# Performance work log

Hardware: AMD Instinct MI355X
Metric: run time of the kernel (lower is better)

The kernel has to match this reference:

```python
import jax, jax.numpy as jnp
import numpy as np
import math

D_MODEL = 1024
H = 16
D_H = D_MODEL // H
B, T = 1, 4096


def setup_inputs() -> dict:
    key = jax.random.key(0)
    ks = jax.random.split(key, 9)
    s = 1.0 / math.sqrt(D_MODEL)
    return {
        "x": jax.random.normal(ks[0], (B, T, D_MODEL), dtype=jnp.float32),
        "W_q": jax.random.normal(ks[1], (D_MODEL, D_MODEL), dtype=jnp.float32) * s,
        "b_q": jax.random.normal(ks[2], (D_MODEL,), dtype=jnp.float32) * 0.01,
        "W_k": jax.random.normal(ks[3], (D_MODEL, D_MODEL), dtype=jnp.float32) * s,
        "b_k": jax.random.normal(ks[4], (D_MODEL,), dtype=jnp.float32) * 0.01,
        "W_v": jax.random.normal(ks[5], (D_MODEL, D_MODEL), dtype=jnp.float32) * s,
        "b_v": jax.random.normal(ks[6], (D_MODEL,), dtype=jnp.float32) * 0.01,
        "W_o": jax.random.normal(ks[7], (D_MODEL, D_MODEL), dtype=jnp.float32) * s,
        "b_o": jax.random.normal(ks[8], (D_MODEL,), dtype=jnp.float32) * 0.01,
    }


def reference(x, W_q, b_q, W_k, b_k, W_v, b_v, W_o, b_o):
    b, t, _ = x.shape
    # torch nn.Linear: y = x @ W.T + b
    Q = x @ W_q.T + b_q  # (B, T, d_model)
    K = x @ W_k.T + b_k
    V = x @ W_v.T + b_v
    # split heads -> (B, h, T, d_h)
    Q = Q.reshape(b, t, H, D_H).transpose(0, 2, 1, 3)
    K = K.reshape(b, t, H, D_H).transpose(0, 2, 1, 3)
    V = V.reshape(b, t, H, D_H).transpose(0, 2, 1, 3)
    # scores (B, h, T, T)
    S = jnp.einsum("bhqd,bhkd->bhqk", Q, K) / math.sqrt(D_H)
    # causal mask: disallow k > q
    causal = jnp.tril(jnp.ones((t, t), dtype=bool))  # True = keep
    S = jnp.where(causal, S, -jnp.inf)
    A = jax.nn.softmax(S, axis=-1)
    Y = jnp.einsum("bhqk,bhkd->bhqd", A, V)  # (B, h, T, d_h)
    Y = Y.transpose(0, 2, 1, 3).reshape(b, t, D_MODEL)
    return Y @ W_o.T + b_o
```

## Files before the change

kernel.cpp:

```cpp
#include <hip/hip_runtime.h>


#define TSZ 4096
#define DM  1024
#define NH  16
#define DH  64
#define QSCALE 0.18033688f

typedef __bf16 bf16x8 __attribute__((ext_vector_type(8)));
typedef float  f32x4  __attribute__((ext_vector_type(4)));

__device__ __forceinline__ unsigned short f2bf(float x) {
    __bf16 h = (__bf16)x;
    return __builtin_bit_cast(unsigned short, h);
}

__device__ __forceinline__ uint4 pack8(const float4 a, const float4 b) {
    uint4 r;
    r.x = (unsigned)f2bf(a.x) | ((unsigned)f2bf(a.y) << 16);
    r.y = (unsigned)f2bf(a.z) | ((unsigned)f2bf(a.w) << 16);
    r.z = (unsigned)f2bf(b.x) | ((unsigned)f2bf(b.y) << 16);
    r.w = (unsigned)f2bf(b.z) | ((unsigned)f2bf(b.w) << 16);
    return r;
}

__device__ __forceinline__ int sw(int row, int cb) {
    return row * 64 + ((cb ^ ((row & 7) << 4)) >> 1);
}

__device__ __forceinline__ void gll16(const unsigned short* g, unsigned short* l) {
    __builtin_amdgcn_global_load_lds((const __attribute__((address_space(1))) void*)g,
                                     (__attribute__((address_space(3))) void*)l,
                                     16, 0, 0);
}

#define XN  4194304u
#define WN  1048576u
__global__ __launch_bounds__(256)
void cvt_kernel(const float* __restrict__ x,  const float* __restrict__ wq,
                const float* __restrict__ wk, const float* __restrict__ wv,
                const float* __restrict__ wo,
                unsigned short* __restrict__ xb,  unsigned short* __restrict__ wqb,
                unsigned short* __restrict__ wkb, unsigned short* __restrict__ wvb,
                unsigned short* __restrict__ wob) {
    size_t e = ((size_t)blockIdx.x * 256 + threadIdx.x) * 8;
    const float* src; unsigned short* dst; size_t off;
    if (e < XN)               { src = x;  dst = xb;  off = e; }
    else if (e < XN + WN)     { src = wq; dst = wqb; off = e - XN; }
    else if (e < XN + 2 * WN) { src = wk; dst = wkb; off = e - XN - WN; }
    else if (e < XN + 3 * WN) { src = wv; dst = wvb; off = e - XN - 2 * WN; }
    else                      { src = wo; dst = wob; off = e - XN - 3 * WN; }
    float4 a = *reinterpret_cast<const float4*>(src + off);
    float4 b = *reinterpret_cast<const float4*>(src + off + 4);
    *reinterpret_cast<uint4*>(dst + off) = pack8(a, b);
}

__global__ __launch_bounds__(256)
void qkv_kernel(const unsigned short* __restrict__ xb,
                const unsigned short* __restrict__ wqb,
                const unsigned short* __restrict__ wkb,
                const unsigned short* __restrict__ wvb,
                const float* __restrict__ bq, const float* __restrict__ bk,
                const float* __restrict__ bv,
                unsigned short* __restrict__ qw,
                unsigned short* __restrict__ kw,
                unsigned short* __restrict__ vtw) {
    const int L = blockIdx.x;
    const int xcd = L & 7, i = L >> 3;
    const int lbx = i % 3, by = i / 3;
    const int bx = xcd * 3 + lbx;
    const int z = bx >> 3;
    const int col0 = (bx & 7) * 128;
    const int row0 = by * 128;

    const unsigned short* W = (z == 0) ? wqb : (z == 1) ? wkb : wvb;
    const float* bias = (z == 0) ? bq : (z == 1) ? bk : bv;
    unsigned short* outp = (z == 0) ? qw : (z == 1) ? kw : vtw;
    const float scale = (z == 0) ? QSCALE : 1.0f;

    __shared__ unsigned short Al[128 * 64];
    __shared__ unsigned short Bl[128 * 64];

    const int tid = threadIdx.x;
    const int wid = tid >> 6, lane = tid & 63, g = lane >> 4, l15 = lane & 15;
    const int wr = (wid >> 1) * 64, wc = (wid & 1) * 64;

    f32x4 acc[4][4];
#pragma unroll
    for (int m = 0; m < 4; ++m)
#pragma unroll
        for (int n = 0; n < 4; ++n) acc[m][n] = (f32x4){0.f, 0.f, 0.f, 0.f};

    const int r_ = tid >> 3, c8_ = tid & 7;
    const int cbyte = (c8_ * 16) ^ ((r_ & 7) << 4);
    const unsigned short* ga0 = xb + (size_t)(row0 + r_) * DM + (cbyte >> 1);
    const unsigned short* gb0 = W + (size_t)(col0 + r_) * DM + (cbyte >> 1);
    unsigned short* la0 = &Al[(size_t)(wid * 64) * 8];
    unsigned short* lb0 = &Bl[(size_t)(wid * 64) * 8];

    for (int kt = 0; kt < DM; kt += 64) {
#pragma unroll
        for (int is = 0; is < 4; ++is) {
            gll16(ga0 + (size_t)(is * 32) * DM + kt, la0 + (size_t)(is * 256) * 8);
            gll16(gb0 + (size_t)(is * 32) * DM + kt, lb0 + (size_t)(is * 256) * 8);
        }
        __syncthreads();
#pragma unroll
        for (int kk = 0; kk < 2; ++kk) {
            bf16x8 a[4], b[4];
#pragma unroll
            for (int m = 0; m < 4; ++m)
                a[m] = *reinterpret_cast<const bf16x8*>(&Al[sw(wr + m * 16 + l15, kk * 64 + 16 * g)]);
#pragma unroll
            for (int n = 0; n < 4; ++n)
                b[n] = *reinterpret_cast<const bf16x8*>(&Bl[sw(wc + n * 16 + l15, kk * 64 + 16 * g)]);
            if (z == 2) {
#pragma unroll
                for (int m = 0; m < 4; ++m)
#pragma unroll
                    for (int n = 0; n < 4; ++n)
                        acc[m][n] = __builtin_amdgcn_mfma_f32_16x16x32_bf16(b[n], a[m], acc[m][n], 0, 0, 0);
            } else {
#pragma unroll
                for (int m = 0; m < 4; ++m)
#pragma unroll
                    for (int n = 0; n < 4; ++n)
                        acc[m][n] = __builtin_amdgcn_mfma_f32_16x16x32_bf16(a[m], b[n], acc[m][n], 0, 0, 0);
            }
        }
        __syncthreads();
    }

    if (z == 2) {
#pragma unroll
        for (int n = 0; n < 4; ++n)
#pragma unroll
            for (int r = 0; r < 4; ++r) {
                int ch = col0 + wc + n * 16 + 4 * g + r;
                float bval = bias[ch];
#pragma unroll
                for (int m = 0; m < 4; ++m) {
                    int t = row0 + wr + m * 16 + l15;
                    outp[(size_t)ch * TSZ + t] = f2bf(acc[m][n][r] + bval);
                }
            }
    } else {
#pragma unroll
        for (int n = 0; n < 4; ++n) {
            int col = col0 + wc + n * 16 + l15;
            float bval = bias[col];
            int hh = col >> 6, dd = col & 63;
#pragma unroll
            for (int m = 0; m < 4; ++m) {
                int rbase = row0 + wr + m * 16 + 4 * g;
#pragma unroll
                for (int r = 0; r < 4; ++r)
                    outp[((size_t)hh * TSZ + rbase + r) * DH + dd] = f2bf((acc[m][n][r] + bval) * scale);
            }
        }
    }
}

__global__ __launch_bounds__(256)
void attn_kernel(const unsigned short* __restrict__ qw,
                 const unsigned short* __restrict__ kw,
                 const unsigned short* __restrict__ vtw,
                 unsigned short* __restrict__ yw) {
    __shared__ unsigned short Qs[64 * 64];
    __shared__ unsigned short Ks[2][64 * 64];
    __shared__ unsigned short Vs[2][64 * 64];
    __shared__ unsigned short Ps[64 * 64];

    const int L = blockIdx.x;
    const int xcd = L & 7, k = L >> 3;
    const int h = xcd + 8 * (k & 1);
    const int qt = 63 - (k >> 1);
    const int tid = threadIdx.x;
    const int wid = tid >> 6, lane = tid & 63, g = lane >> 4, l15 = lane & 15;

    const unsigned short* qbase = qw + (size_t)h * TSZ * DH;
    const unsigned short* kbase = kw + (size_t)h * TSZ * DH;
    const unsigned short* vbase = vtw + (size_t)h * DH * TSZ;

    {
        const unsigned short* qsrc = qbase + (size_t)qt * 64 * DH;
#pragma unroll
        for (int i2 = 0; i2 < 2; ++i2) {
            int c = tid + i2 * 256;
            int r = c >> 3, c8 = c & 7;
            *reinterpret_cast<uint4*>(&Qs[sw(r, c8 * 16)]) =
                *reinterpret_cast<const uint4*>(qsrc + c * 8);
            *reinterpret_cast<uint4*>(&Ks[0][sw(r, c8 * 16)]) =
                *reinterpret_cast<const uint4*>(kbase + c * 8);
            *reinterpret_cast<uint4*>(&Vs[0][sw(r, c8 * 16)]) =
                *reinterpret_cast<const uint4*>(vbase + (size_t)r * TSZ + c8 * 8);
        }
    }
    __syncthreads();

    bf16x8 aq[2];
    aq[0] = *reinterpret_cast<const bf16x8*>(&Qs[sw(wid * 16 + l15, 16 * g)]);
    aq[1] = *reinterpret_cast<const bf16x8*>(&Qs[sw(wid * 16 + l15, 64 + 16 * g)]);

    float l_st = 0.f;
    f32x4 accO[4];
#pragma unroll
    for (int n = 0; n < 4; ++n) accO[n] = (f32x4){0.f, 0.f, 0.f, 0.f};

    for (int j = 0; j <= qt; ++j) {
        const int cur = j & 1;
        const bool pf = (j < qt);
        uint4 pk0, pk1, pv0, pv1;
        if (pf) {
            const unsigned short* ks = kbase + (size_t)(j + 1) * 64 * DH;
            const unsigned short* vs = vbase + (size_t)(j + 1) * 64;
            int c0 = tid, c1 = tid + 256;
            pk0 = *reinterpret_cast<const uint4*>(ks + c0 * 8);
            pk1 = *reinterpret_cast<const uint4*>(ks + c1 * 8);
            pv0 = *reinterpret_cast<const uint4*>(vs + (size_t)(c0 >> 3) * TSZ + (c0 & 7) * 8);
            pv1 = *reinterpret_cast<const uint4*>(vs + (size_t)(c1 >> 3) * TSZ + (c1 & 7) * 8);
        }

        f32x4 sacc[4];
#pragma unroll
        for (int n = 0; n < 4; ++n) sacc[n] = (f32x4){0.f, 0.f, 0.f, 0.f};
        __builtin_amdgcn_s_setprio(1);
#pragma unroll
        for (int kk = 0; kk < 2; ++kk) {
#pragma unroll
            for (int n = 0; n < 4; ++n) {
                bf16x8 bk = *reinterpret_cast<const bf16x8*>(&Ks[cur][sw(n * 16 + l15, kk * 64 + 16 * g)]);
                sacc[n] = __builtin_amdgcn_mfma_f32_16x16x32_bf16(bk, aq[kk], sacc[n], 0, 0, 0);
            }
        }
        __builtin_amdgcn_s_setprio(0);
        if (j == qt) {
#pragma unroll
            for (int n = 0; n < 4; ++n)
#pragma unroll
                for (int r = 0; r < 4; ++r)
                    if (n * 16 + 4 * g + r > wid * 16 + l15) sacc[n][r] = -__builtin_inff();
        }

        float p[4][4];
#pragma unroll
        for (int n = 0; n < 4; ++n) {
#pragma unroll
            for (int r = 0; r < 4; ++r) { p[n][r] = exp2f(sacc[n][r]); l_st += p[n][r]; }
        }

#pragma unroll
        for (int n = 0; n < 4; ++n)
#pragma unroll
            for (int s = 0; s < 2; ++s) {
                unsigned pk32;
                asm("v_cvt_pk_bf16_f32 %0, %1, %2"
                    : "=v"(pk32) : "v"(p[n][2 * s]), "v"(p[n][2 * s + 1]));
                *reinterpret_cast<unsigned*>(
                    &Ps[sw(wid * 16 + l15, (16 * n + 4 * g + 2 * s) * 2)]) = pk32;
            }

        if (pf) {
            int c0 = tid, c1 = tid + 256;
            *reinterpret_cast<uint4*>(&Ks[cur ^ 1][sw(c0 >> 3, (c0 & 7) * 16)]) = pk0;
            *reinterpret_cast<uint4*>(&Ks[cur ^ 1][sw(c1 >> 3, (c1 & 7) * 16)]) = pk1;
            *reinterpret_cast<uint4*>(&Vs[cur ^ 1][sw(c0 >> 3, (c0 & 7) * 16)]) = pv0;
            *reinterpret_cast<uint4*>(&Vs[cur ^ 1][sw(c1 >> 3, (c1 & 7) * 16)]) = pv1;
        }

        __builtin_amdgcn_s_setprio(1);
#pragma unroll
        for (int kk = 0; kk < 2; ++kk) {
            bf16x8 pa = *reinterpret_cast<const bf16x8*>(&Ps[sw(wid * 16 + l15, kk * 64 + 16 * g)]);
#pragma unroll
            for (int n = 0; n < 4; ++n) {
                bf16x8 bv = *reinterpret_cast<const bf16x8*>(&Vs[cur][sw(n * 16 + l15, kk * 64 + 16 * g)]);
                accO[n] = __builtin_amdgcn_mfma_f32_16x16x32_bf16(pa, bv, accO[n], 0, 0, 0);
            }
        }
        __builtin_amdgcn_s_setprio(0);
        __syncthreads();
    }

    float ltot = l_st;
    ltot += __shfl_xor(ltot, 16);
    ltot += __shfl_xor(ltot, 32);
    float* Lbuf = reinterpret_cast<float*>(Ps);
    if (lane < 16) Lbuf[wid * 16 + lane] = ltot;
#pragma unroll
    for (int r = 0; r < 4; ++r) {
        float inv = 1.0f / Lbuf[wid * 16 + 4 * g + r];
        int row = qt * 64 + wid * 16 + 4 * g + r;
#pragma unroll
        for (int n = 0; n < 4; ++n)
            yw[(size_t)row * DM + h * DH + n * 16 + l15] = f2bf(accO[n][r] * inv);
    }
}

__global__ __launch_bounds__(256)
void oproj_kernel(const unsigned short* __restrict__ y,
                  const unsigned short* __restrict__ wob,
                  const float* __restrict__ bo,
                  float* __restrict__ out) {
    const int L = blockIdx.x;
    const int xcd = L & 7, i = L >> 3;
    const int bx = i & 7, lby = i >> 3;
    const int by = xcd * 4 + lby;
    const int row0 = by * 128, col0 = bx * 128;

    __shared__ unsigned short Al[128 * 64];
    __shared__ unsigned short Bl[128 * 64];

    const int tid = threadIdx.x;
    const int wid = tid >> 6, lane = tid & 63, g = lane >> 4, l15 = lane & 15;
    const int wr = (wid >> 1) * 64, wc = (wid & 1) * 64;

    f32x4 acc[4][4];
#pragma unroll
    for (int m = 0; m < 4; ++m)
#pragma unroll
        for (int n = 0; n < 4; ++n) acc[m][n] = (f32x4){0.f, 0.f, 0.f, 0.f};

    const int r_ = tid >> 3, c8_ = tid & 7;
    const int cbyte = (c8_ * 16) ^ ((r_ & 7) << 4);
    const unsigned short* ga0 = y + (size_t)(row0 + r_) * DM + (cbyte >> 1);
    const unsigned short* gb0 = wob + (size_t)(col0 + r_) * DM + (cbyte >> 1);
    unsigned short* la0 = &Al[(size_t)(wid * 64) * 8];
    unsigned short* lb0 = &Bl[(size_t)(wid * 64) * 8];

    for (int kt = 0; kt < DM; kt += 64) {
#pragma unroll
        for (int is = 0; is < 4; ++is) {
            gll16(ga0 + (size_t)(is * 32) * DM + kt, la0 + (size_t)(is * 256) * 8);
            gll16(gb0 + (size_t)(is * 32) * DM + kt, lb0 + (size_t)(is * 256) * 8);
        }
        __syncthreads();
#pragma unroll
        for (int kk = 0; kk < 2; ++kk) {
            bf16x8 a[4], b[4];
#pragma unroll
            for (int m = 0; m < 4; ++m)
                a[m] = *reinterpret_cast<const bf16x8*>(&Al[sw(wr + m * 16 + l15, kk * 64 + 16 * g)]);
#pragma unroll
            for (int n = 0; n < 4; ++n)
                b[n] = *reinterpret_cast<const bf16x8*>(&Bl[sw(wc + n * 16 + l15, kk * 64 + 16 * g)]);
#pragma unroll
            for (int m = 0; m < 4; ++m)
#pragma unroll
                for (int n = 0; n < 4; ++n)
                    acc[m][n] = __builtin_amdgcn_mfma_f32_16x16x32_bf16(a[m], b[n], acc[m][n], 0, 0, 0);
        }
        __syncthreads();
    }

#pragma unroll
    for (int n = 0; n < 4; ++n) {
        int col = col0 + wc + n * 16 + l15;
        float bval = bo[col];
#pragma unroll
        for (int m = 0; m < 4; ++m) {
            int rbase = row0 + wr + m * 16 + 4 * g;
#pragma unroll
            for (int r = 0; r < 4; ++r)
                out[(size_t)(rbase + r) * DM + col] = acc[m][n][r] + bval;
        }
    }
}

extern "C" void kernel_launch(void* const* d_in, const int* in_sizes, int n_in,
                              void* d_out, int out_size, void* d_ws, size_t ws_size,
                              hipStream_t stream) {
    const float* x  = (const float*)d_in[0];
    const float* Wq = (const float*)d_in[1];
    const float* bq = (const float*)d_in[2];
    const float* Wk = (const float*)d_in[3];
    const float* bk = (const float*)d_in[4];
    const float* Wv = (const float*)d_in[5];
    const float* bv = (const float*)d_in[6];
    const float* Wo = (const float*)d_in[7];
    const float* bo = (const float*)d_in[8];
    float* out = (float*)d_out;

    unsigned short* xb  = (unsigned short*)d_ws;
    unsigned short* wqb = xb + 4194304;
    unsigned short* wkb = wqb + 1048576;
    unsigned short* wvb = wkb + 1048576;
    unsigned short* wob = wvb + 1048576;
    unsigned short* qw  = wob + 1048576;
    unsigned short* kw  = qw + 4194304;
    unsigned short* vtw = kw + 4194304;
    unsigned short* yw  = xb;

    cvt_kernel<<<4096, 256, 0, stream>>>(x, Wq, Wk, Wv, Wo, xb, wqb, wkb, wvb, wob);
    qkv_kernel<<<768, 256, 0, stream>>>(xb, wqb, wkb, wvb, bq, bk, bv, qw, kw, vtw);
    attn_kernel<<<1024, 256, 0, stream>>>(qw, kw, vtw, yw);
    oproj_kernel<<<256, 256, 0, stream>>>(yw, wob, bo, out);
}
```

Before: 137.3 us.

## Halve attention block to two waves with 32 query rows each and async K/V loads

The attention kernel now runs with 128 threads. Each wave handles two 16-row query fragments, so every K and V fragment read from LDS feeds two MFMAs, which halves LDS reads per FLOP. The K/V prefetch uses gll16 (global-to-LDS direct loads) with a precomputed swizzled offset instead of staging through registers. The Q buffer is dropped by reusing Ps, which lowers LDS use. In exchange there are fewer waves per block to hide latency, each thread holds more accumulator registers, and more global loads are issued per thread.

```diff
diff --git a/kernel.cpp b/kernel.cpp
--- a/kernel.cpp
+++ b/kernel.cpp
@@ -161,12 +161,11 @@
     }
 }
 
-__global__ __launch_bounds__(256)
+__global__ __launch_bounds__(128)
 void attn_kernel(const unsigned short* __restrict__ qw,
                  const unsigned short* __restrict__ kw,
                  const unsigned short* __restrict__ vtw,
                  unsigned short* __restrict__ yw) {
-    __shared__ unsigned short Qs[64 * 64];
     __shared__ unsigned short Ks[2][64 * 64];
     __shared__ unsigned short Vs[2][64 * 64];
     __shared__ unsigned short Ps[64 * 64];
@@ -182,13 +181,23 @@
     const unsigned short* kbase = kw + (size_t)h * TSZ * DH;
     const unsigned short* vbase = vtw + (size_t)h * DH * TSZ;
 
+    const int cbase = wid * 256;
+    int kloff[4]; size_t vloff[4];
+#pragma unroll
+    for (int i2 = 0; i2 < 4; ++i2) {
+        int c = cbase + i2 * 64 + lane;
+        int r = c >> 3, cc = (c & 7) ^ (r & 7);
+        kloff[i2] = r * 64 + cc * 8;
+        vloff[i2] = (size_t)r * TSZ + cc * 8;
+    }
+
     {
         const unsigned short* qsrc = qbase + (size_t)qt * 64 * DH;
 #pragma unroll
-        for (int i2 = 0; i2 < 2; ++i2) {
-            int c = tid + i2 * 256;
+        for (int i2 = 0; i2 < 4; ++i2) {
+            int c = tid + i2 * 128;
             int r = c >> 3, c8 = c & 7;
-            *reinterpret_cast<uint4*>(&Qs[sw(r, c8 * 16)]) =
+            *reinterpret_cast<uint4*>(&Ps[sw(r, c8 * 16)]) =
                 *reinterpret_cast<const uint4*>(qsrc + c * 8);
             *reinterpret_cast<uint4*>(&Ks[0][sw(r, c8 * 16)]) =
                 *reinterpret_cast<const uint4*>(kbase + c * 8);
@@ -198,103 +207,114 @@
     }
     __syncthreads();
 
-    bf16x8 aq[2];
-    aq[0] = *reinterpret_cast<const bf16x8*>(&Qs[sw(wid * 16 + l15, 16 * g)]);
-    aq[1] = *reinterpret_cast<const bf16x8*>(&Qs[sw(wid * 16 + l15, 64 + 16 * g)]);
-
-    float l_st = 0.f;
-    f32x4 accO[4];
-#pragma unroll
-    for (int n = 0; n < 4; ++n) accO[n] = (f32x4){0.f, 0.f, 0.f, 0.f};
+    bf16x8 aq[2][2];
+#pragma unroll
+    for (int f = 0; f < 2; ++f)
+#pragma unroll
+        for (int kk = 0; kk < 2; ++kk)
+            aq[f][kk] = *reinterpret_cast<const bf16x8*>(
+                &Ps[sw(wid * 32 + 16 * f + l15, kk * 64 + 16 * g)]);
+    __syncthreads();
+
+    float l_st[2] = {0.f, 0.f};
+    f32x4 accO[2][4];
+#pragma unroll
+    for (int f = 0; f < 2; ++f)
+#pragma unroll
+        for (int n = 0; n < 4; ++n) accO[f][n] = (f32x4){0.f, 0.f, 0.f, 0.f};
 
     for (int j = 0; j <= qt; ++j) {
         const int cur = j & 1;
-        const bool pf = (j < qt);
-        uint4 pk0, pk1, pv0, pv1;
-        if (pf) {
+        if (j < qt) {
             const unsigned short* ks = kbase + (size_t)(j + 1) * 64 * DH;
             const unsigned short* vs = vbase + (size_t)(j + 1) * 64;
-            int c0 = tid, c1 = tid + 256;
-            pk0 = *reinterpret_cast<const uint4*>(ks + c0 * 8);
-            pk1 = *reinterpret_cast<const uint4*>(ks + c1 * 8);
-            pv0 = *reinterpret_cast<const uint4*>(vs + (size_t)(c0 >> 3) * TSZ + (c0 & 7) * 8);
-            pv1 = *reinterpret_cast<const uint4*>(vs + (size_t)(c1 >> 3) * TSZ + (c1 & 7) * 8);
-        }
-
-        f32x4 sacc[4];
-#pragma unroll
-        for (int n = 0; n < 4; ++n) sacc[n] = (f32x4){0.f, 0.f, 0.f, 0.f};
+            unsigned short* kb = &Ks[cur ^ 1][cbase * 8];
+            unsigned short* vb = &Vs[cur ^ 1][cbase * 8];
+#pragma unroll
+            for (int i2 = 0; i2 < 4; ++i2) {
+                gll16(ks + kloff[i2], kb + i2 * 512);
+                gll16(vs + vloff[i2], vb + i2 * 512);
+            }
+        }
+
+        f32x4 sacc[2][4];
+#pragma unroll
+        for (int f = 0; f < 2; ++f)
+#pragma unroll
+            for (int n = 0; n < 4; ++n) sacc[f][n] = (f32x4){0.f, 0.f, 0.f, 0.f};
         __builtin_amdgcn_s_setprio(1);
 #pragma unroll
         for (int kk = 0; kk < 2; ++kk) {
 #pragma unroll
             for (int n = 0; n < 4; ++n) {
                 bf16x8 bk = *reinterpret_cast<const bf16x8*>(&Ks[cur][sw(n * 16 + l15, kk * 64 + 16 * g)]);
-                sacc[n] = __builtin_amdgcn_mfma_f32_16x16x32_bf16(bk, aq[kk], sacc[n], 0, 0, 0);
+                sacc[0][n] = __builtin_amdgcn_mfma_f32_16x16x32_bf16(bk, aq[0][kk], sacc[0][n], 0, 0, 0);
+                sacc[1][n] = __builtin_amdgcn_mfma_f32_16x16x32_bf16(bk, aq[1][kk], sacc[1][n], 0, 0, 0);
             }
         }
         __builtin_amdgcn_s_setprio(0);
         if (j == qt) {
 #pragma unroll
-            for (int n = 0; n < 4; ++n)
-#pragma unroll
-                for (int r = 0; r < 4; ++r)
-                    if (n * 16 + 4 * g + r > wid * 16 + l15) sacc[n][r] = -__builtin_inff();
-        }
-
-        float p[4][4];
-#pragma unroll
-        for (int n = 0; n < 4; ++n) {
-#pragma unroll
-            for (int r = 0; r < 4; ++r) { p[n][r] = exp2f(sacc[n][r]); l_st += p[n][r]; }
-        }
-
-#pragma unroll
-        for (int n = 0; n < 4; ++n)
-#pragma unroll
-            for (int s = 0; s < 2; ++s) {
-                unsigned pk32;
-                asm("v_cvt_pk_bf16_f32 %0, %1, %2"
-                    : "=v"(pk32) : "v"(p[n][2 * s]), "v"(p[n][2 * s + 1]));
-                *reinterpret_cast<unsigned*>(
-                    &Ps[sw(wid * 16 + l15, (16 * n + 4 * g + 2 * s) * 2)]) = pk32;
-            }
-
-        if (pf) {
-            int c0 = tid, c1 = tid + 256;
-            *reinterpret_cast<uint4*>(&Ks[cur ^ 1][sw(c0 >> 3, (c0 & 7) * 16)]) = pk0;
-            *reinterpret_cast<uint4*>(&Ks[cur ^ 1][sw(c1 >> 3, (c1 & 7) * 16)]) = pk1;
-            *reinterpret_cast<uint4*>(&Vs[cur ^ 1][sw(c0 >> 3, (c0 & 7) * 16)]) = pv0;
-            *reinterpret_cast<uint4*>(&Vs[cur ^ 1][sw(c1 >> 3, (c1 & 7) * 16)]) = pv1;
-        }
+            for (int f = 0; f < 2; ++f)
+#pragma unroll
+                for (int n = 0; n < 4; ++n)
+#pragma unroll
+                    for (int r = 0; r < 4; ++r)
+                        if (n * 16 + 4 * g + r > wid * 32 + 16 * f + l15)
+                            sacc[f][n][r] = -__builtin_inff();
+        }
+
+#pragma unroll
+        for (int f = 0; f < 2; ++f)
+#pragma unroll
+            for (int n = 0; n < 4; ++n) {
+                float p0 = exp2f(sacc[f][n][0]);
+                float p1 = exp2f(sacc[f][n][1]);
+                float p2 = exp2f(sacc[f][n][2]);
+                float p3 = exp2f(sacc[f][n][3]);
+                l_st[f] += (p0 + p1) + (p2 + p3);
+                unsigned w0, w1;
+                asm("v_cvt_pk_bf16_f32 %0, %1, %2" : "=v"(w0) : "v"(p0), "v"(p1));
+                asm("v_cvt_pk_bf16_f32 %0, %1, %2" : "=v"(w1) : "v"(p2), "v"(p3));
+                int prow = wid * 32 + 16 * f + l15;
+                *reinterpret_cast<unsigned*>(&Ps[sw(prow, (16 * n + 4 * g) * 2)]) = w0;
+                *reinterpret_cast<unsigned*>(&Ps[sw(prow, (16 * n + 4 * g + 2) * 2)]) = w1;
+            }
 
         __builtin_amdgcn_s_setprio(1);
 #pragma unroll
         for (int kk = 0; kk < 2; ++kk) {
-            bf16x8 pa = *reinterpret_cast<const bf16x8*>(&Ps[sw(wid * 16 + l15, kk * 64 + 16 * g)]);
+            bf16x8 pa0 = *reinterpret_cast<const bf16x8*>(&Ps[sw(wid * 32 + l15, kk * 64 + 16 * g)]);
+            bf16x8 pa1 = *reinterpret_cast<const bf16x8*>(&Ps[sw(wid * 32 + 16 + l15, kk * 64 + 16 * g)]);
 #pragma unroll
             for (int n = 0; n < 4; ++n) {
                 bf16x8 bv = *reinterpret_cast<const bf16x8*>(&Vs[cur][sw(n * 16 + l15, kk * 64 + 16 * g)]);
-                accO[n] = __builtin_amdgcn_mfma_f32_16x16x32_bf16(pa, bv, accO[n], 0, 0, 0);
+                accO[0][n] = __builtin_amdgcn_mfma_f32_16x16x32_bf16(pa0, bv, accO[0][n], 0, 0, 0);
+                accO[1][n] = __builtin_amdgcn_mfma_f32_16x16x32_bf16(pa1, bv, accO[1][n], 0, 0, 0);
             }
         }
         __builtin_amdgcn_s_setprio(0);
         __syncthreads();
     }
 
-    float ltot = l_st;
-    ltot += __shfl_xor(ltot, 16);
-    ltot += __shfl_xor(ltot, 32);
     float* Lbuf = reinterpret_cast<float*>(Ps);
-    if (lane < 16) Lbuf[wid * 16 + lane] = ltot;
-#pragma unroll
-    for (int r = 0; r < 4; ++r) {
-        float inv = 1.0f / Lbuf[wid * 16 + 4 * g + r];
-        int row = qt * 64 + wid * 16 + 4 * g + r;
-#pragma unroll
-        for (int n = 0; n < 4; ++n)
-            yw[(size_t)row * DM + h * DH + n * 16 + l15] = f2bf(accO[n][r] * inv);
-    }
+#pragma unroll
+    for (int f = 0; f < 2; ++f) {
+        float lt = l_st[f];
+        lt += __shfl_xor(lt, 16);
+        lt += __shfl_xor(lt, 32);
+        if (lane < 16) Lbuf[wid * 32 + 16 * f + lane] = lt;
+    }
+#pragma unroll
+    for (int f = 0; f < 2; ++f)
+#pragma unroll
+        for (int r = 0; r < 4; ++r) {
+            float inv = 1.0f / Lbuf[wid * 32 + 16 * f + 4 * g + r];
+            int row = qt * 64 + wid * 32 + 16 * f + 4 * g + r;
+#pragma unroll
+            for (int n = 0; n < 4; ++n)
+                yw[(size_t)row * DM + h * DH + n * 16 + l15] = f2bf(accO[f][n][r] * inv);
+        }
 }
 
 __global__ __launch_bounds__(256)
@@ -393,6 +413,6 @@
 
     cvt_kernel<<<4096, 256, 0, stream>>>(x, Wq, Wk, Wv, Wo, xb, wqb, wkb, wvb, wob);
     qkv_kernel<<<768, 256, 0, stream>>>(xb, wqb, wkb, wvb, bq, bk, bv, qw, kw, vtw);
-    attn_kernel<<<1024, 256, 0, stream>>>(qw, kw, vtw, yw);
+    attn_kernel<<<1024, 128, 0, stream>>>(qw, kw, vtw, yw);
     oproj_kernel<<<256, 256, 0, stream>>>(yw, wob, bo, out);
 }
```

New measurement: 175.3 us. 1.28x slower.
